# Kernel optimization log

Hardware: AMD Instinct MI355X
Metric: run time of the kernel (lower is better)

Reference implementation:

```python
import jax, jax.numpy as jnp
import numpy as np

DIM, HEADS, HD = 1536, 12, 128
B, F, H, W = 1, 8, 16, 28
L = F * H * W  # 3584
EPS = 1e-6


def setup_inputs() -> dict:
    key = jax.random.key(0)
    ks = jax.random.split(key, 8)
    s = 0.02
    x = jax.random.normal(ks[0], (B, L, DIM), jnp.float32)
    # RoPE tables: angles pos * theta_j, shape [1024, HD//2]
    ang = jnp.arange(1024, dtype=jnp.float32)[:, None] / (
        10000.0 ** (jnp.arange(HD // 2, dtype=jnp.float32) / (HD // 2)))
    freqs_cos = jnp.cos(ang)
    freqs_sin = jnp.sin(ang)
    Wq = jax.random.normal(ks[1], (DIM, DIM), jnp.float32) * s
    Wk = jax.random.normal(ks[2], (DIM, DIM), jnp.float32) * s
    Wv = jax.random.normal(ks[3], (DIM, DIM), jnp.float32) * s
    Wo = jax.random.normal(ks[4], (DIM, DIM), jnp.float32) * s
    zb = jnp.zeros((DIM,), jnp.float32)
    return dict(x=x, freqs_cos=freqs_cos, freqs_sin=freqs_sin,
                Wq=Wq, bq=zb, Wk=Wk, bk=zb, Wv=Wv, bv=zb, Wo=Wo, bo=zb,
                gq=jnp.ones((DIM,), jnp.float32), gk=jnp.ones((DIM,), jnp.float32),
                f=F, h=H, w=W)


def rms_norm(t, g, eps=EPS):
    # WanRMSNorm: x * rsqrt(mean(x^2) + eps) * weight, over last dim (full `dim`)
    return t * jax.lax.rsqrt(jnp.mean(t * t, axis=-1, keepdims=True) + eps) * g


def rope_apply(t, f, h, w, cos, sin):
    # t: [B, L, H, D]; 3D rope with per-axis frequency splits [c-2(c//3), c//3, c//3]
    B_, L_, H_, D_ = t.shape
    c = D_ // 2
    s0 = c - 2 * (c // 3)
    s1 = c // 3

    def build(tab):
        tf = jnp.broadcast_to(tab[:f, :s0][:, None, None, :], (f, h, w, s0))
        th = jnp.broadcast_to(tab[:h, s0:s0 + s1][None, :, None, :], (f, h, w, s1))
        tw = jnp.broadcast_to(tab[:w, s0 + s1:c][None, None, :, :], (f, h, w, s1))
        return jnp.concatenate([tf, th, tw], axis=-1).reshape(f * h * w, c)[:L_]

    cs = build(cos)[None, :, None, :]  # [1, L, 1, c]
    sn = build(sin)[None, :, None, :]
    tp = t.reshape(B_, L_, H_, c, 2)   # consecutive pairs -> complex (re, im)
    tr, ti = tp[..., 0], tp[..., 1]
    out_r = tr * cs - ti * sn
    out_i = tr * sn + ti * cs
    return jnp.stack([out_r, out_i], axis=-1).reshape(B_, L_, H_, D_)


def reference(x, freqs_cos, freqs_sin, Wq, bq, Wk, bk, Wv, bv, Wo, bo, gq, gk, f, h, w):
    B_, L_, _ = x.shape
    q = rms_norm(x @ Wq.T + bq, gq).reshape(B_, L_, HEADS, HD)
    k = rms_norm(x @ Wk.T + bk, gk).reshape(B_, L_, HEADS, HD)
    v = (x @ Wv.T + bv).reshape(B_, L_, HEADS, HD)
    q = rope_apply(q, f, h, w, freqs_cos, freqs_sin)
    k = rope_apply(k, f, h, w, freqs_cos, freqs_sin)
    scale = 1.0 / np.sqrt(HD).astype(np.float32)
    att = jax.nn.softmax(jnp.einsum('bqhd,bkhd->bhqk', q, k) * scale, axis=-1)
    o = jnp.einsum('bhqk,bkhd->bqhd', att, v).reshape(B_, L_, DIM)
    return o @ Wo.T + bo
```

## Files before the change

### kernel.cpp

```cpp
#include <hip/hip_runtime.h>
#include <hip/hip_bf16.h>


#define DIM   1536
#define HEADS 12
#define HD    128
#define LSEQ  3584

typedef __bf16 bf16_t;
typedef __attribute__((ext_vector_type(8))) __bf16 bf16x8;
typedef __attribute__((ext_vector_type(4))) float f32x4;
typedef __attribute__((ext_vector_type(16))) float f32x16;
typedef unsigned int u32;
typedef __attribute__((ext_vector_type(2))) unsigned int u32x2;
typedef __attribute__((ext_vector_type(4))) unsigned int u32x4;

static __device__ __forceinline__ ushort f2bf(float f) {
  bf16_t h = (bf16_t)f;
  return __builtin_bit_cast(ushort, h);
}
static __device__ __forceinline__ float bf2f(ushort u) {
  return (float)__builtin_bit_cast(bf16_t, u);
}
static __device__ __forceinline__ u32 pkbf(float a, float b) {
  return (u32)f2bf(a) | ((u32)f2bf(b) << 16);
}

static __device__ __forceinline__ void plswap(u32& x, u32& y, int hi) {
#if __has_builtin(__builtin_amdgcn_permlane32_swap)
  (void)hi;
  u32x2 r = __builtin_amdgcn_permlane32_swap(x, y, false, false);
  x = r[0]; y = r[1];
#else
  u32 sx = __shfl_xor(x, 32, 64);
  u32 sy = __shfl_xor(y, 32, 64);
  u32 nx = hi ? sy : x;
  u32 ny = hi ? y : sx;
  x = nx; y = ny;
#endif
}

__global__ __launch_bounds__(256) void cvt_f32_bf16(const float* __restrict__ in,
                                                    ushort* __restrict__ out, int n) {
  int i = (blockIdx.x * 256 + threadIdx.x) * 4;
  if (i + 3 < n) {
    float4 v = *reinterpret_cast<const float4*>(in + i);
    ushort4 o;
    o.x = f2bf(v.x); o.y = f2bf(v.y); o.z = f2bf(v.z); o.w = f2bf(v.w);
    *reinterpret_cast<ushort4*>(out + i) = o;
  }
}

__global__ __launch_bounds__(256) void cvt_w4(const float* __restrict__ s0,
                                              const float* __restrict__ s1,
                                              const float* __restrict__ s2,
                                              const float* __restrict__ s3,
                                              ushort* __restrict__ dst) {
  const int WD4 = (DIM * DIM) / 4;
  const int per = WD4 / 256;
  int mat = blockIdx.x / per;
  int rb  = blockIdx.x % per;
  const float* s = mat == 0 ? s0 : (mat == 1 ? s1 : (mat == 2 ? s2 : s3));
  int i = (rb * 256 + threadIdx.x) * 4;
  float4 v = *reinterpret_cast<const float4*>(s + i);
  ushort4 o;
  o.x = f2bf(v.x); o.y = f2bf(v.y); o.z = f2bf(v.z); o.w = f2bf(v.w);
  *reinterpret_cast<ushort4*>(dst + (size_t)mat * DIM * DIM + i) = o;
}

template <int SEGS, bool OUT_F32>
__global__ __launch_bounds__(256) void gemm_bt(const ushort* __restrict__ A,
                                               const ushort* __restrict__ B,
                                               const float* __restrict__ bias0,
                                               const float* __restrict__ bias1,
                                               const float* __restrict__ bias2,
                                               void* __restrict__ Cout) {
  const int K = DIM;
  const int MT = LSEQ / 128;
  const int ntiles = MT * (SEGS * DIM / 128);
  __shared__ __attribute__((aligned(16))) ushort As[128 * 32];
  __shared__ __attribute__((aligned(16))) ushort Bs[128 * 32];
  const int tid  = threadIdx.x;
  const int lane = tid & 63;
  const int wid  = tid >> 6;
  const int wm = (wid >> 1) * 64;
  const int wn = (wid & 1) * 64;
  const int lr = lane & 15;
  const int lg = lane >> 4;
  const int crow = lane >> 2;
  const int ccol = (lane & 3) * 8;

  for (int tile = blockIdx.x; tile < ntiles; tile += gridDim.x) {
    const int m0 = (tile % MT) * 128;
    const int n0 = (tile / MT) * 128;

    f32x4 acc[4][4] = {};

    for (int kt = 0; kt < K; kt += 32) {
      __syncthreads();
#pragma unroll
      for (int i = 0; i < 2; ++i) {
        int chunk = wid * 2 + i;
        int row = chunk * 16 + crow;
        const ushort* ga = A + (size_t)(m0 + row) * K + kt + ccol;
        const ushort* gb = B + (size_t)(n0 + row) * K + kt + ccol;
        __builtin_amdgcn_global_load_lds(
            (__attribute__((address_space(1))) void*)(void*)ga,
            (__attribute__((address_space(3))) void*)(&As[chunk * 512]), 16, 0, 0);
        __builtin_amdgcn_global_load_lds(
            (__attribute__((address_space(1))) void*)(void*)gb,
            (__attribute__((address_space(3))) void*)(&Bs[chunk * 512]), 16, 0, 0);
      }
      __syncthreads();

      bf16x8 af[4], bfr[4];
#pragma unroll
      for (int m = 0; m < 4; ++m)
        af[m] = *reinterpret_cast<const bf16x8*>(&As[(wm + m * 16 + lr) * 32 + lg * 8]);
#pragma unroll
      for (int n = 0; n < 4; ++n)
        bfr[n] = *reinterpret_cast<const bf16x8*>(&Bs[(wn + n * 16 + lr) * 32 + lg * 8]);
#pragma unroll
      for (int m = 0; m < 4; ++m)
#pragma unroll
        for (int n = 0; n < 4; ++n)
          acc[m][n] = __builtin_amdgcn_mfma_f32_16x16x32_bf16(af[m], bfr[n], acc[m][n], 0, 0, 0);
    }

    int seg = 0;
    const float* bp = bias0;
    if (SEGS == 3) {
      seg = n0 >= 2 * DIM ? 2 : (n0 >= DIM ? 1 : 0);
      bp = seg == 0 ? bias0 : (seg == 1 ? bias1 : bias2);
    }
    const int nbase = n0 - seg * DIM;

#pragma unroll
    for (int m = 0; m < 4; ++m) {
#pragma unroll
      for (int n = 0; n < 4; ++n) {
        int col = nbase + wn + n * 16 + lr;
        float bvv = bp[col];
#pragma unroll
        for (int r = 0; r < 4; ++r) {
          int row = m0 + wm + m * 16 + lg * 4 + r;
          float v = acc[m][n][r] + bvv;
          if (OUT_F32)
            ((float*)Cout)[(size_t)row * DIM + col] = v;
          else
            ((ushort*)Cout)[(size_t)seg * ((size_t)LSEQ * DIM) + (size_t)row * DIM + col] = f2bf(v);
        }
      }
    }
    __syncthreads();
  }
}

__global__ __launch_bounds__(256) void normrope(ushort* __restrict__ Qb,
                                                ushort* __restrict__ Kb,
                                                const float* __restrict__ gq,
                                                const float* __restrict__ gk,
                                                const float* __restrict__ cosT,
                                                const float* __restrict__ sinT) {
  __shared__ float red[4];
  const int l = blockIdx.x;
  const int tid = threadIdx.x;
  ushort* row = (blockIdx.y == 0 ? Qb : Kb) + (size_t)l * DIM;
  const float* g = blockIdx.y == 0 ? gq : gk;

  const u32* rp = reinterpret_cast<const u32*>(row);
  u32 pk[3];
  float v[6];
#pragma unroll
  for (int i = 0; i < 3; ++i) {
    pk[i] = rp[tid * 3 + i];
    v[2 * i]     = bf2f((ushort)(pk[i] & 0xffff));
    v[2 * i + 1] = bf2f((ushort)(pk[i] >> 16));
  }
  float ss = 0.f;
#pragma unroll
  for (int i = 0; i < 6; ++i) ss += v[i] * v[i];
#pragma unroll
  for (int off = 1; off < 64; off <<= 1) ss += __shfl_xor(ss, off, 64);
  if ((tid & 63) == 0) red[tid >> 6] = ss;
  __syncthreads();
  float tot = red[0] + red[1] + red[2] + red[3];
  float rms = rsqrtf(tot * (1.0f / DIM) + 1e-6f);

  const int fi = l / 448;
  const int rem = l % 448;
  const int hi = rem / 28;
  const int wi = rem % 28;

  u32* wp = reinterpret_cast<u32*>(row);
#pragma unroll
  for (int i = 0; i < 3; ++i) {
    int p = tid * 3 + i;
    int head = p >> 6;
    int j = p & 63;
    int trow = (j < 22) ? fi : ((j < 43) ? hi : wi);
    float cv = cosT[trow * 64 + j];
    float sv = sinT[trow * 64 + j];
    int idx = head * 128 + 2 * j;
    float xr = v[2 * i] * rms * g[idx];
    float xi = v[2 * i + 1] * rms * g[idx + 1];
    float orr = xr * cv - xi * sv;
    float oii = xr * sv + xi * cv;
    wp[p] = (u32)f2bf(orr) | ((u32)f2bf(oii) << 16);
  }
}

#define QBLK 128
#define KVB  64

__global__ __launch_bounds__(256, 2) void attn(const ushort* __restrict__ Q,
                                               const ushort* __restrict__ Kp,
                                               const ushort* __restrict__ Vp,
                                               ushort* __restrict__ O,
                                               float* __restrict__ Opart,
                                               float* __restrict__ mlbuf) {
  __shared__ __attribute__((aligned(16))) ushort Ks[2][KVB * 128];
  __shared__ __attribute__((aligned(16))) ushort Vt[2][128][72];
  const int tid  = threadIdx.x;
  const int lane = tid & 63;
  const int wv   = tid >> 6;
  const int lq   = lane & 31;
  const int hi   = lane >> 5;
  const int h    = blockIdx.y;
  const int q0   = blockIdx.x * QBLK;
  const float scale = 0.08838834764831845f;

  const int split  = blockIdx.z;
  const int nsplit = gridDim.z;
  const int NT     = LSEQ / KVB;
  const int t_lo   = split * NT / nsplit;
  const int t_hi   = (split + 1) * NT / nsplit;

  bf16x8 qf[8];
  {
    const ushort* qbase = Q + (size_t)(q0 + wv * 32 + lq) * DIM + h * HD;
#pragma unroll
    for (int d = 0; d < 8; ++d)
      qf[d] = *reinterpret_cast<const bf16x8*>(qbase + d * 16 + hi * 8);
  }

  f32x16 accO[4] = {};
  float m = -1e30f, lsum = 0.f;

  const int mbk = tid >> 4;
  const int mbd = tid & 15;

  uint4 vr0, vr1, vr2, vr3;
  auto issueK = [&](int t, int nb) {
    const int kv0 = t * KVB;
#pragma unroll
    for (int i = 0; i < 4; ++i) {
      int o16 = (wv * 4 + i) * 64 + lane;
      int r = o16 >> 4;
      int b = (o16 & 15) * 16;
      int srcu = (b ^ ((r & 7) << 4)) >> 1;
      const ushort* gp = Kp + (size_t)(kv0 + r) * DIM + h * HD + srcu;
      __builtin_amdgcn_global_load_lds(
          (__attribute__((address_space(1))) void*)(void*)gp,
          (__attribute__((address_space(3))) void*)(&Ks[nb][(wv * 4 + i) * 512]), 16, 0, 0);
    }
  };
  auto loadV = [&](int t) {
    const ushort* vbase = Vp + (size_t)(t * KVB + mbk * 4) * DIM + h * HD + mbd * 8;
    vr0 = *reinterpret_cast<const uint4*>(vbase);
    vr1 = *reinterpret_cast<const uint4*>(vbase + DIM);
    vr2 = *reinterpret_cast<const uint4*>(vbase + 2 * DIM);
    vr3 = *reinterpret_cast<const uint4*>(vbase + 3 * DIM);
  };
  auto writeV = [&](int nb) {
    const ushort* s0 = reinterpret_cast<const ushort*>(&vr0);
    const ushort* s1 = reinterpret_cast<const ushort*>(&vr1);
    const ushort* s2 = reinterpret_cast<const ushort*>(&vr2);
    const ushort* s3 = reinterpret_cast<const ushort*>(&vr3);
#pragma unroll
    for (int jj = 0; jj < 8; ++jj) {
      int j = (jj + mbd) & 7;
      uint2 w;
      w.x = (u32)s0[j] | ((u32)s1[j] << 16);
      w.y = (u32)s2[j] | ((u32)s3[j] << 16);
      *reinterpret_cast<uint2*>(&Vt[nb][mbd * 8 + j][mbk * 4]) = w;
    }
  };

  issueK(t_lo, 0);
  loadV(t_lo);

  int buf = 0;
  for (int t = t_lo; t < t_hi; ++t) {
    writeV(buf);
    __syncthreads();

    if (t + 1 < t_hi) {
      issueK(t + 1, buf ^ 1);
      loadV(t + 1);
    }

    f32x16 sv0 = {}, sv1 = {};
    __builtin_amdgcn_s_setprio(1);
#pragma unroll
    for (int d = 0; d < 8; ++d) {
      int db = d * 32 + hi * 16;
      const bf16x8 a0 = *reinterpret_cast<const bf16x8*>(
          (const char*)&Ks[buf][0] + lq * 256 + (db ^ ((lq & 7) << 4)));
      const bf16x8 a1 = *reinterpret_cast<const bf16x8*>(
          (const char*)&Ks[buf][0] + (32 + lq) * 256 + (db ^ ((lq & 7) << 4)));
      sv0 = __builtin_amdgcn_mfma_f32_32x32x16_bf16(a0, qf[d], sv0, 0, 0, 0);
      sv1 = __builtin_amdgcn_mfma_f32_32x32x16_bf16(a1, qf[d], sv1, 0, 0, 0);
    }
    __builtin_amdgcn_s_setprio(0);

#pragma unroll
    for (int hf = 0; hf < 2; ++hf) {
      const f32x16& sv = hf == 0 ? sv0 : sv1;

      float t01 = fmaxf(sv[0], sv[1]),   t23 = fmaxf(sv[2], sv[3]);
      float t45 = fmaxf(sv[4], sv[5]),   t67 = fmaxf(sv[6], sv[7]);
      float t89 = fmaxf(sv[8], sv[9]),   tab = fmaxf(sv[10], sv[11]);
      float tcd = fmaxf(sv[12], sv[13]), tef = fmaxf(sv[14], sv[15]);
      float q0m = fmaxf(fmaxf(t01, t23), fmaxf(t45, t67));
      float q1m = fmaxf(fmaxf(t89, tab), fmaxf(tcd, tef));
      float pmax = fmaxf(q0m, q1m);
      pmax = fmaxf(pmax, __shfl_xor(pmax, 32, 64));
      pmax *= scale;

      if (__any(pmax > m + 8.f)) {
        float mn = fmaxf(m, pmax);
        float al = __expf(m - mn);
        m = mn;
        lsum *= al;
#pragma unroll
        for (int r = 0; r < 16; ++r) {
          int qr = (r & 3) + 8 * (r >> 2) + 4 * hi;
          float alr = __shfl(al, qr, 64);
          accO[0][r] *= alr; accO[1][r] *= alr;
          accO[2][r] *= alr; accO[3][r] *= alr;
        }
      }

      float p[16];
      float psum = 0.f;
#pragma unroll
      for (int r = 0; r < 16; ++r) {
        p[r] = __expf(fmaf(sv[r], scale, -m));
        psum += p[r];
      }
      psum += __shfl_xor(psum, 32, 64);
      lsum += psum;

      u32 a0 = pkbf(p[0], p[1]),   a1 = pkbf(p[2], p[3]);
      u32 a4 = pkbf(p[4], p[5]),   a5 = pkbf(p[6], p[7]);
      u32 c0 = pkbf(p[8], p[9]),   c1 = pkbf(p[10], p[11]);
      u32 c4 = pkbf(p[12], p[13]), c5 = pkbf(p[14], p[15]);
      plswap(a0, a4, hi);
      plswap(a1, a5, hi);
      plswap(c0, c4, hi);
      plswap(c1, c5, hi);
      u32x4 w0 = {a0, a1, a4, a5};
      u32x4 w1 = {c0, c1, c4, c5};
      bf16x8 pa0 = __builtin_bit_cast(bf16x8, w0);
      bf16x8 pa1 = __builtin_bit_cast(bf16x8, w1);

      __builtin_amdgcn_s_setprio(1);
#pragma unroll
      for (int nd = 0; nd < 4; ++nd) {
        bf16x8 vb0 = *reinterpret_cast<const bf16x8*>(
            &Vt[buf][nd * 32 + lq][hf * 32 + hi * 8]);
        accO[nd] = __builtin_amdgcn_mfma_f32_32x32x16_bf16(pa0, vb0, accO[nd], 0, 0, 0);
      }
#pragma unroll
      for (int nd = 0; nd < 4; ++nd) {
        bf16x8 vb1 = *reinterpret_cast<const bf16x8*>(
            &Vt[buf][nd * 32 + lq][hf * 32 + 16 + hi * 8]);
        accO[nd] = __builtin_amdgcn_mfma_f32_32x32x16_bf16(pa1, vb1, accO[nd], 0, 0, 0);
      }
      __builtin_amdgcn_s_setprio(0);
    }

    __syncthreads();
    buf ^= 1;
  }

  if (gridDim.z == 1) {
    float inv_own = 1.0f / lsum;
#pragma unroll
    for (int r = 0; r < 16; ++r) {
      int qr = (r & 3) + 8 * (r >> 2) + 4 * hi;
      float inv = __shfl(inv_own, qr, 64);
      ushort* orow = O + (size_t)(q0 + wv * 32 + qr) * DIM + h * HD;
#pragma unroll
      for (int nd = 0; nd < 4; ++nd)
        orow[nd * 32 + lq] = f2bf(accO[nd][r] * inv);
    }
  } else {
    float* Op = Opart + ((size_t)split * HEADS + h) * ((size_t)LSEQ * HD);
#pragma unroll
    for (int r = 0; r < 16; ++r) {
      int qr = (r & 3) + 8 * (r >> 2) + 4 * hi;
      float* orow = Op + (size_t)(q0 + wv * 32 + qr) * HD;
#pragma unroll
      for (int nd = 0; nd < 4; ++nd)
        orow[nd * 32 + lq] = accO[nd][r];
    }
    if (hi == 0) {
      size_t row = (size_t)split * (HEADS * LSEQ) + (size_t)h * LSEQ + (q0 + wv * 32 + lq);
      mlbuf[2 * row]     = m;
      mlbuf[2 * row + 1] = lsum;
    }
  }
}

__global__ __launch_bounds__(256) void attn_merge(const float* __restrict__ Opart,
                                                  const float* __restrict__ mlbuf,
                                                  ushort* __restrict__ Ob, int nsplit) {
  const int RN = HEADS * LSEQ;
  int gi = blockIdx.x * 256 + threadIdx.x;
  int row = gi >> 5;
  int d4 = (gi & 31) * 4;
  if (row >= RN) return;
  int h = row / LSEQ, q = row % LSEQ;

  float M = -1e30f;
  for (int s = 0; s < nsplit; ++s) M = fmaxf(M, mlbuf[2 * ((size_t)s * RN + row)]);
  float den = 0.f;
  float4 acc = {0.f, 0.f, 0.f, 0.f};
  for (int s = 0; s < nsplit; ++s) {
    float ms = mlbuf[2 * ((size_t)s * RN + row)];
    float ls = mlbuf[2 * ((size_t)s * RN + row) + 1];
    float w = __expf(ms - M);
    den += ls * w;
    const float4 o = *reinterpret_cast<const float4*>(
        &Opart[((size_t)s * RN + row) * HD + d4]);
    acc.x += w * o.x; acc.y += w * o.y; acc.z += w * o.z; acc.w += w * o.w;
  }
  float inv = 1.0f / den;
  ushort4 r;
  r.x = f2bf(acc.x * inv); r.y = f2bf(acc.y * inv);
  r.z = f2bf(acc.z * inv); r.w = f2bf(acc.w * inv);
  *reinterpret_cast<ushort4*>(&Ob[(size_t)q * DIM + h * HD + d4]) = r;
}

extern "C" void kernel_launch(void* const* d_in, const int* in_sizes, int n_in,
                              void* d_out, int out_size, void* d_ws, size_t ws_size,
                              hipStream_t stream) {
  (void)in_sizes; (void)n_in; (void)out_size;
  const float* x    = (const float*)d_in[0];
  const float* cosT = (const float*)d_in[1];
  const float* sinT = (const float*)d_in[2];
  const float* Wq   = (const float*)d_in[3];
  const float* bq   = (const float*)d_in[4];
  const float* Wk   = (const float*)d_in[5];
  const float* bk   = (const float*)d_in[6];
  const float* Wv   = (const float*)d_in[7];
  const float* bv_in = (const float*)d_in[8];
  const float* Wo   = (const float*)d_in[9];
  const float* bo   = (const float*)d_in[10];
  const float* gq   = (const float*)d_in[11];
  const float* gk   = (const float*)d_in[12];

  const size_t LD = (size_t)LSEQ * DIM;
  const size_t WD = (size_t)DIM * DIM;
  const size_t base_bytes = (5 * LD + 4 * WD) * sizeof(ushort);
  if (ws_size < base_bytes) return;

  ushort* xb  = (ushort*)d_ws;
  ushort* Wqb = xb + LD;
  ushort* Wob = Wqb + 3 * WD;
  ushort* Qb  = Wob + WD;
  ushort* Kb  = Qb + LD;
  ushort* Vb  = Kb + LD;
  ushort* Ob  = Vb + LD;

  const size_t RN = (size_t)HEADS * LSEQ;
  const size_t split_bytes = RN * HD * 4 + RN * 8;
  int nsplit = 1;
  if (ws_size >= base_bytes + 3 * split_bytes) nsplit = 3;
  else if (ws_size >= base_bytes + 2 * split_bytes) nsplit = 2;
  float* Opart = (float*)((char*)d_ws + base_bytes);
  float* mlbuf = Opart + (size_t)nsplit * RN * HD;

  cvt_f32_bf16<<<(int)(LD / 4 / 256), 256, 0, stream>>>(x, xb, (int)LD);
  cvt_w4<<<(int)(4 * WD / 4 / 256), 256, 0, stream>>>(Wq, Wk, Wv, Wo, Wqb);

  {
    int nt = (LSEQ / 128) * (3 * DIM / 128);
    gemm_bt<3, false><<<nt < 768 ? nt : 768, 256, 0, stream>>>(
        xb, Wqb, bq, bk, bv_in, Qb);
  }

  normrope<<<dim3(LSEQ, 2), 256, 0, stream>>>(Qb, Kb, gq, gk, cosT, sinT);

  attn<<<dim3(LSEQ / QBLK, HEADS, nsplit), 256, 0, stream>>>(Qb, Kb, Vb, Ob, Opart, mlbuf);
  if (nsplit > 1)
    attn_merge<<<(int)(RN * 32 / 256), 256, 0, stream>>>(Opart, mlbuf, Ob, nsplit);

  {
    int nt = (LSEQ / 128) * (DIM / 128);
    gemm_bt<1, true><<<nt < 768 ? nt : 768, 256, 0, stream>>>(
        Ob, Wob, bo, bo, bo, d_out);
  }
}
```

Before: 304.4 us.

## Double GEMM K-tile to 64 with XOR-swizzled LDS and split attention QK per half

The projection GEMM now stages 64-wide K slices into LDS with an XOR swizzle, which halves the number of barrier-separated iterations and avoids LDS bank conflicts on fragment reads. In the attention kernel, the QK^T MFMA for each 32-key half is computed right before that half's softmax instead of both halves up front. The intent is to cut live registers and to overlap the second half's MFMAs with the first half's softmax. Doubling the LDS tiles raises shared memory per block, which may lower occupancy, and the serialized max reduction is slightly longer.

```diff
diff --git a/kernel.cpp b/kernel.cpp
--- a/kernel.cpp
+++ b/kernel.cpp
@@ -78,8 +78,8 @@
   const int K = DIM;
   const int MT = LSEQ / 128;
   const int ntiles = MT * (SEGS * DIM / 128);
-  __shared__ __attribute__((aligned(16))) ushort As[128 * 32];
-  __shared__ __attribute__((aligned(16))) ushort Bs[128 * 32];
+  __shared__ __attribute__((aligned(16))) ushort As[128 * 64];
+  __shared__ __attribute__((aligned(16))) ushort Bs[128 * 64];
   const int tid  = threadIdx.x;
   const int lane = tid & 63;
   const int wid  = tid >> 6;
@@ -87,8 +87,9 @@
   const int wn = (wid & 1) * 64;
   const int lr = lane & 15;
   const int lg = lane >> 4;
-  const int crow = lane >> 2;
-  const int ccol = (lane & 3) * 8;
+  const int srow = lane >> 3;
+  const int sbyte = (lane & 7) * 16;
+  const int ssrc = (sbyte ^ (srow << 4)) >> 1;
 
   for (int tile = blockIdx.x; tile < ntiles; tile += gridDim.x) {
     const int m0 = (tile % MT) * 128;
@@ -96,14 +97,14 @@
 
     f32x4 acc[4][4] = {};
 
-    for (int kt = 0; kt < K; kt += 32) {
+    for (int kt = 0; kt < K; kt += 64) {
       __syncthreads();
 #pragma unroll
-      for (int i = 0; i < 2; ++i) {
-        int chunk = wid * 2 + i;
-        int row = chunk * 16 + crow;
-        const ushort* ga = A + (size_t)(m0 + row) * K + kt + ccol;
-        const ushort* gb = B + (size_t)(n0 + row) * K + kt + ccol;
+      for (int i = 0; i < 4; ++i) {
+        int chunk = wid * 4 + i;
+        int row = chunk * 8 + srow;
+        const ushort* ga = A + (size_t)(m0 + row) * K + kt + ssrc;
+        const ushort* gb = B + (size_t)(n0 + row) * K + kt + ssrc;
         __builtin_amdgcn_global_load_lds(
             (__attribute__((address_space(1))) void*)(void*)ga,
             (__attribute__((address_space(3))) void*)(&As[chunk * 512]), 16, 0, 0);
@@ -113,18 +114,28 @@
       }
       __syncthreads();
 
-      bf16x8 af[4], bfr[4];
-#pragma unroll
-      for (int m = 0; m < 4; ++m)
-        af[m] = *reinterpret_cast<const bf16x8*>(&As[(wm + m * 16 + lr) * 32 + lg * 8]);
-#pragma unroll
-      for (int n = 0; n < 4; ++n)
-        bfr[n] = *reinterpret_cast<const bf16x8*>(&Bs[(wn + n * 16 + lr) * 32 + lg * 8]);
-#pragma unroll
-      for (int m = 0; m < 4; ++m)
-#pragma unroll
-        for (int n = 0; n < 4; ++n)
-          acc[m][n] = __builtin_amdgcn_mfma_f32_16x16x32_bf16(af[m], bfr[n], acc[m][n], 0, 0, 0);
+#pragma unroll
+      for (int kk = 0; kk < 2; ++kk) {
+        bf16x8 af[4], bfr[4];
+        const int cb = lg * 16 + kk * 64;
+#pragma unroll
+        for (int m = 0; m < 4; ++m) {
+          int row = wm + m * 16 + lr;
+          af[m] = *reinterpret_cast<const bf16x8*>(
+              (const char*)As + row * 128 + (cb ^ ((row & 7) << 4)));
+        }
+#pragma unroll
+        for (int n = 0; n < 4; ++n) {
+          int row = wn + n * 16 + lr;
+          bfr[n] = *reinterpret_cast<const bf16x8*>(
+              (const char*)Bs + row * 128 + (cb ^ ((row & 7) << 4)));
+        }
+#pragma unroll
+        for (int m = 0; m < 4; ++m)
+#pragma unroll
+          for (int n = 0; n < 4; ++n)
+            acc[m][n] = __builtin_amdgcn_mfma_f32_16x16x32_bf16(af[m], bfr[n], acc[m][n], 0, 0, 0);
+      }
     }
 
     int seg = 0;
@@ -300,31 +311,22 @@
       loadV(t + 1);
     }
 
-    f32x16 sv0 = {}, sv1 = {};
-    __builtin_amdgcn_s_setprio(1);
-#pragma unroll
-    for (int d = 0; d < 8; ++d) {
-      int db = d * 32 + hi * 16;
-      const bf16x8 a0 = *reinterpret_cast<const bf16x8*>(
-          (const char*)&Ks[buf][0] + lq * 256 + (db ^ ((lq & 7) << 4)));
-      const bf16x8 a1 = *reinterpret_cast<const bf16x8*>(
-          (const char*)&Ks[buf][0] + (32 + lq) * 256 + (db ^ ((lq & 7) << 4)));
-      sv0 = __builtin_amdgcn_mfma_f32_32x32x16_bf16(a0, qf[d], sv0, 0, 0, 0);
-      sv1 = __builtin_amdgcn_mfma_f32_32x32x16_bf16(a1, qf[d], sv1, 0, 0, 0);
-    }
-    __builtin_amdgcn_s_setprio(0);
-
 #pragma unroll
     for (int hf = 0; hf < 2; ++hf) {
-      const f32x16& sv = hf == 0 ? sv0 : sv1;
-
-      float t01 = fmaxf(sv[0], sv[1]),   t23 = fmaxf(sv[2], sv[3]);
-      float t45 = fmaxf(sv[4], sv[5]),   t67 = fmaxf(sv[6], sv[7]);
-      float t89 = fmaxf(sv[8], sv[9]),   tab = fmaxf(sv[10], sv[11]);
-      float tcd = fmaxf(sv[12], sv[13]), tef = fmaxf(sv[14], sv[15]);
-      float q0m = fmaxf(fmaxf(t01, t23), fmaxf(t45, t67));
-      float q1m = fmaxf(fmaxf(t89, tab), fmaxf(tcd, tef));
-      float pmax = fmaxf(q0m, q1m);
+      f32x16 sv = {};
+      __builtin_amdgcn_s_setprio(1);
+#pragma unroll
+      for (int d = 0; d < 8; ++d) {
+        int db = d * 32 + hi * 16;
+        const bf16x8 a = *reinterpret_cast<const bf16x8*>(
+            (const char*)&Ks[buf][0] + (hf * 32 + lq) * 256 + (db ^ ((lq & 7) << 4)));
+        sv = __builtin_amdgcn_mfma_f32_32x32x16_bf16(a, qf[d], sv, 0, 0, 0);
+      }
+      __builtin_amdgcn_s_setprio(0);
+
+      float pmax = sv[0];
+#pragma unroll
+      for (int r = 1; r < 16; ++r) pmax = fmaxf(pmax, sv[r]);
       pmax = fmaxf(pmax, __shfl_xor(pmax, 32, 64));
       pmax *= scale;
 
```

Result: faster. 286.7 us (-5.8%).
